# Performance work log

Measured on AMD Instinct MI355X. Metric: run time of the kernel, lower is better.

The kernel has to match this reference:

```python
import jax, jax.numpy as jnp
import numpy as np

N_NODES = 100000
F_DIM = 128
D_LAT = 64
N_EDGES = 1000000
H_DIM = 128


def setup_inputs() -> dict:
    key = jax.random.key(0)
    ks = jax.random.split(key, 10)
    rng = np.random.default_rng(0)
    # positive edges (random graph) and non-edge negative pairs (dedup vs edge set,
    # mirroring the membership check in the torch elbo loop)
    edges = rng.integers(0, N_NODES, size=(2, N_EDGES))
    edge_hash = edges[0].astype(np.int64) * N_NODES + edges[1]
    cand = rng.integers(0, N_NODES, size=(2, 2 * N_EDGES))
    cand_hash = cand[0].astype(np.int64) * N_NODES + cand[1]
    keep = ~np.isin(cand_hash, edge_hash)
    neg = cand[:, keep][:, :N_EDGES]
    r = lambda k, s, sc=1.0: jax.random.normal(k, s, jnp.float32) * sc
    return {
        "x": r(ks[0], (N_NODES, F_DIM)),
        "eps": r(ks[1], (N_NODES, D_LAT)),
        "W_mu": r(ks[2], (F_DIM, D_LAT), 0.05),
        "b_mu": jnp.zeros((D_LAT,), jnp.float32),
        "W_lv": r(ks[3], (F_DIM, D_LAT), 0.05),
        "b_lv": jnp.zeros((D_LAT,), jnp.float32),
        "W1": r(ks[4], (D_LAT, H_DIM), 0.1),
        "b1": jnp.zeros((H_DIM,), jnp.float32),
        "W2": r(ks[5], (H_DIM, 1), 0.1),
        "b2": jnp.zeros((1,), jnp.float32),
        "edge_index": jnp.asarray(edges, jnp.int64) if jax.config.jax_enable_x64 else jnp.asarray(edges, jnp.int32),
        "neg_index": jnp.asarray(neg, jnp.int64) if jax.config.jax_enable_x64 else jnp.asarray(neg, jnp.int32),
    }


def reference(x, eps, W_mu, b_mu, W_lv, b_lv, W1, b1, W2, b2, edge_index, neg_index):
    # encoder: per-node diagonal Gaussian q(z|x)
    mu = x @ W_mu + b_mu            # [N, D]
    logvar = x @ W_lv + b_lv        # [N, D]
    z = mu + eps * jnp.exp(0.5 * logvar)  # q.rsample()

    def pair_logits(idx):
        zu = z[idx[0]]              # [E, D] gather
        zv = z[idx[1]]
        h = jax.nn.relu((zu * zv) @ W1 + b1)  # [E, H]
        return (h @ W2 + b2)[:, 0]  # [E]

    # Bernoulli(logits).log_prob(1) = log_sigmoid(l); log(1 - sigmoid(l)) = log_sigmoid(-l)
    true_lp = jax.nn.log_sigmoid(pair_logits(edge_index))
    false_lp = jax.nn.log_sigmoid(-pair_logits(neg_index))
    recon = jnp.mean(jnp.concatenate([true_lp, false_lp]))

    # KL(q || N(0, I)) per node, mean over nodes
    kl = jnp.mean(0.5 * jnp.sum(jnp.square(mu) + jnp.exp(logvar) - 1.0 - logvar, axis=-1))
    return -(recon - kl)
```

## Files before the change

### kernel.cpp

```cpp
#include <hip/hip_runtime.h>
#include <math.h>

#define F_DIM 128
#define D_LAT 64
#define H_DIM 128

typedef __attribute__((ext_vector_type(8))) short bf16x8;
typedef __attribute__((ext_vector_type(4))) float f32x4;
typedef __attribute__((ext_vector_type(2))) float f32x2;
typedef __attribute__((ext_vector_type(2))) unsigned long long u64x2;

__device__ __forceinline__ unsigned short f2bf(float f) {
    unsigned int u = __builtin_bit_cast(unsigned int, f);
    return (unsigned short)((u + 0x8000u) >> 16);
}

__device__ __forceinline__ long prod_fp8(unsigned long long qu, unsigned long long qv) {
    const unsigned int ul = (unsigned int)qu, uh = (unsigned int)(qu >> 32);
    const unsigned int vl = (unsigned int)qv, vh = (unsigned int)(qv >> 32);
    const f32x2 u01 = __builtin_amdgcn_cvt_pk_f32_fp8(ul, false);
    const f32x2 u23 = __builtin_amdgcn_cvt_pk_f32_fp8(ul, true);
    const f32x2 u45 = __builtin_amdgcn_cvt_pk_f32_fp8(uh, false);
    const f32x2 u67 = __builtin_amdgcn_cvt_pk_f32_fp8(uh, true);
    const f32x2 v01 = __builtin_amdgcn_cvt_pk_f32_fp8(vl, false);
    const f32x2 v23 = __builtin_amdgcn_cvt_pk_f32_fp8(vl, true);
    const f32x2 v45 = __builtin_amdgcn_cvt_pk_f32_fp8(vh, false);
    const f32x2 v67 = __builtin_amdgcn_cvt_pk_f32_fp8(vh, true);
    const f32x2 p01 = u01 * v01, p23 = u23 * v23;
    const f32x2 p45 = u45 * v45, p67 = u67 * v67;
    unsigned int r0 = __builtin_amdgcn_cvt_pk_fp8_f32(p01[0], p01[1], 0u, false);
    r0 = __builtin_amdgcn_cvt_pk_fp8_f32(p23[0], p23[1], r0, true);
    unsigned int r1 = __builtin_amdgcn_cvt_pk_fp8_f32(p45[0], p45[1], 0u, false);
    r1 = __builtin_amdgcn_cvt_pk_fp8_f32(p67[0], p67[1], r1, true);
    return (long)(((unsigned long long)r1 << 32) | r0);
}

__global__ __launch_bounds__(256) void enc_mfma_kernel(
    const float* __restrict__ x, const float* __restrict__ eps,
    const float* __restrict__ Wmu, const float* __restrict__ bmu,
    const float* __restrict__ Wlv, const float* __restrict__ blv,
    unsigned char* __restrict__ zb, float* __restrict__ accum, int nNodes)
{
    const int lane = threadIdx.x & 63;
    const int li   = lane & 15;
    const int gi   = lane >> 4;

    bf16x8 wf[8][4];
#pragma unroll
    for (int t = 0; t < 4; ++t)
#pragma unroll
        for (int s = 0; s < 4; ++s)
#pragma unroll
            for (int j = 0; j < 8; ++j) {
                const int k = s * 32 + gi * 8 + j;
                wf[t][s][j]     = (short)f2bf(Wmu[k * D_LAT + 16 * t + li]);
                wf[t + 4][s][j] = (short)f2bf(Wlv[k * D_LAT + 16 * t + li]);
            }
    float bmu4[4], blv4[4];
#pragma unroll
    for (int t = 0; t < 4; ++t) {
        bmu4[t] = bmu[16 * t + li];
        blv4[t] = blv[16 * t + li];
    }

    const int wid = (blockIdx.x * blockDim.x + threadIdx.x) >> 6;
    const int nw  = (gridDim.x * blockDim.x) >> 6;
    const int NB  = nNodes >> 4;

    float klacc = 0.f;
    for (int nb = wid; nb < NB; nb += nw) {
        const int nbase = nb << 4;
        const float* __restrict__ xrow = x + (size_t)(nbase + li) * F_DIM;

        bf16x8 af[4];
#pragma unroll
        for (int s = 0; s < 4; ++s) {
            const f32x4 v0 = *(const f32x4*)(xrow + s * 32 + gi * 8);
            const f32x4 v1 = *(const f32x4*)(xrow + s * 32 + gi * 8 + 4);
#pragma unroll
            for (int j = 0; j < 4; ++j) {
                af[s][j]     = (short)f2bf(v0[j]);
                af[s][j + 4] = (short)f2bf(v1[j]);
            }
        }

        f32x4 acc[8];
#pragma unroll
        for (int t = 0; t < 4; ++t) {
            acc[t]     = (f32x4){bmu4[t], bmu4[t], bmu4[t], bmu4[t]};
            acc[t + 4] = (f32x4){blv4[t], blv4[t], blv4[t], blv4[t]};
        }
#pragma unroll
        for (int t = 0; t < 8; ++t)
#pragma unroll
            for (int s = 0; s < 4; ++s)
                acc[t] = __builtin_amdgcn_mfma_f32_16x16x32_bf16(af[s], wf[t][s], acc[t], 0, 0, 0);

#pragma unroll
        for (int r = 0; r < 4; ++r) {
            const int row = nbase + gi * 4 + r;
#pragma unroll
            for (int t = 0; t < 4; ++t) {
                const float mu  = acc[t][r];
                const float lv  = acc[t + 4][r];
                const float e05 = __expf(0.5f * lv);
                klacc += mu * mu + e05 * e05 - 1.0f - lv;
                const float zv = fmaf(eps[(size_t)row * D_LAT + 16 * t + li], e05, mu);
                zb[(size_t)row * D_LAT + 16 * t + li] =
                    (unsigned char)(__builtin_amdgcn_cvt_pk_fp8_f32(zv, 0.f, 0u, false) & 0xffu);
            }
        }
    }
    for (int off = 32; off; off >>= 1) klacc += __shfl_xor(klacc, off);
    if (lane == 0) atomicAdd(&accum[1], 0.5f * klacc);
}

__global__ __launch_bounds__(256) void edge_mfma_kernel(
    const unsigned char* __restrict__ zb,
    const int* __restrict__ eidx, const int* __restrict__ nidx,
    const float* __restrict__ W1, const float* __restrict__ b1,
    const float* __restrict__ W2, const float* __restrict__ b2,
    float* __restrict__ accum, int E)
{
    const int lane = threadIdx.x & 63;
    const int li   = lane & 15;
    const int gi   = lane >> 4;

    long w1q[8][2];
#pragma unroll
    for (int t = 0; t < 8; ++t)
#pragma unroll
        for (int s = 0; s < 2; ++s) {
            float f[8];
#pragma unroll
            for (int j = 0; j < 8; ++j)
                f[j] = W1[(gi * 16 + s * 8 + j) * H_DIM + 16 * t + li];
            unsigned int r0 = __builtin_amdgcn_cvt_pk_fp8_f32(f[0], f[1], 0u, false);
            r0 = __builtin_amdgcn_cvt_pk_fp8_f32(f[2], f[3], r0, true);
            unsigned int r1 = __builtin_amdgcn_cvt_pk_fp8_f32(f[4], f[5], 0u, false);
            r1 = __builtin_amdgcn_cvt_pk_fp8_f32(f[6], f[7], r1, true);
            w1q[t][s] = (long)(((unsigned long long)r1 << 32) | r0);
        }
    float b1r[8], w2r[8];
#pragma unroll
    for (int t = 0; t < 8; ++t) {
        b1r[t] = b1[16 * t + li];
        w2r[t] = W2[16 * t + li];
    }
    const float b2v = b2[0];

    const int wid = (blockIdx.x * blockDim.x + threadIdx.x) >> 6;
    const int nw  = (gridDim.x * blockDim.x) >> 6;
    const int NBpos = E >> 4;
    const int NBH   = NBpos;

    float lp = 0.f;

    auto load_idx = [&](int hb, int& u0, int& v0, int& u1, int& v1) {
        const int h   = (hb < NBH) ? hb : (NBH - 1);
        const int pb0 = 2 * h, pb1 = 2 * h + 1;
        const int* __restrict__ i0 = (pb0 < NBpos) ? eidx : nidx;
        const int* __restrict__ i1 = (pb1 < NBpos) ? eidx : nidx;
        const int m0 = ((pb0 < NBpos) ? pb0 : pb0 - NBpos) << 4;
        const int m1 = ((pb1 < NBpos) ? pb1 : pb1 - NBpos) << 4;
        u0 = i0[m0 + li]; v0 = i0[E + m0 + li];
        u1 = i1[m1 + li]; v1 = i1[E + m1 + li];
    };
    auto load_row = [&](int node) -> u64x2 {
        return *(const u64x2*)(zb + (size_t)node * D_LAT + (gi << 4));
    };
    auto do_block = [&](u64x2 qu, u64x2 qv, bool pos) {
        const long pa0 = prod_fp8(qu[0], qv[0]);
        const long pa1 = prod_fp8(qu[1], qv[1]);
        f32x4 acc[8];
#pragma unroll
        for (int t = 0; t < 8; ++t)
            acc[t] = (f32x4){b1r[t], b1r[t], b1r[t], b1r[t]};
#pragma unroll
        for (int t = 0; t < 8; ++t) {
            acc[t] = __builtin_amdgcn_mfma_f32_16x16x32_fp8_fp8(pa0, w1q[t][0], acc[t], 0, 0, 0);
            acc[t] = __builtin_amdgcn_mfma_f32_16x16x32_fp8_fp8(pa1, w1q[t][1], acc[t], 0, 0, 0);
        }
        float t0 = 0.f, t1 = 0.f, t2 = 0.f, t3 = 0.f;
#pragma unroll
        for (int t = 0; t < 8; ++t) {
            t0 += fmaxf(acc[t][0], 0.f) * w2r[t];
            t1 += fmaxf(acc[t][1], 0.f) * w2r[t];
            t2 += fmaxf(acc[t][2], 0.f) * w2r[t];
            t3 += fmaxf(acc[t][3], 0.f) * w2r[t];
        }
#pragma unroll
        for (int off = 1; off < 16; off <<= 1) {
            t0 += __shfl_xor(t0, off);
            t1 += __shfl_xor(t1, off);
            t2 += __shfl_xor(t2, off);
            t3 += __shfl_xor(t3, off);
        }
        const float sg = pos ? 1.f : -1.f;
        const float l0 = sg * (t0 + b2v), l1 = sg * (t1 + b2v);
        const float l2 = sg * (t2 + b2v), l3 = sg * (t3 + b2v);
        lp += fminf(l0, 0.f) - __logf(1.f + __expf(-fabsf(l0)));
        lp += fminf(l1, 0.f) - __logf(1.f + __expf(-fabsf(l1)));
        lp += fminf(l2, 0.f) - __logf(1.f + __expf(-fabsf(l2)));
        lp += fminf(l3, 0.f) - __logf(1.f + __expf(-fabsf(l3)));
    };

    int ju0, jv0, ju1, jv1;
    load_idx(wid, ju0, jv0, ju1, jv1);
    u64x2 A0u = load_row(ju0), A0v = load_row(jv0);
    u64x2 A1u = load_row(ju1), A1v = load_row(jv1);
    load_idx(wid + nw, ju0, jv0, ju1, jv1);

#pragma unroll 2
    for (int hb = wid; hb < NBH; hb += nw) {
        u64x2 B0u = load_row(ju0), B0v = load_row(jv0);
        u64x2 B1u = load_row(ju1), B1v = load_row(jv1);
        int ku0, kv0, ku1, kv1;
        load_idx(hb + 2 * nw, ku0, kv0, ku1, kv1);
        do_block(A0u, A0v, 2 * hb < NBpos);
        do_block(A1u, A1v, 2 * hb + 1 < NBpos);
        A0u = B0u; A0v = B0v; A1u = B1u; A1v = B1v;
        ju0 = ku0; jv0 = kv0; ju1 = ku1; jv1 = kv1;
    }

    for (int off = 32; off; off >>= 1) lp += __shfl_xor(lp, off);
    if (lane == 0) atomicAdd(&accum[0], lp * 0.0625f);
}

__global__ void fin_kernel(const float* __restrict__ accum, float* __restrict__ out,
                           int nNodes, int E)
{
    const float recon = accum[0] / (float)(2 * E);
    const float kl    = accum[1] / (float)nNodes;
    out[0] = kl - recon;
}

extern "C" void kernel_launch(void* const* d_in, const int* in_sizes, int n_in,
                              void* d_out, int out_size, void* d_ws, size_t ws_size,
                              hipStream_t stream)
{
    const float* x    = (const float*)d_in[0];
    const float* eps  = (const float*)d_in[1];
    const float* Wmu  = (const float*)d_in[2];
    const float* bmu  = (const float*)d_in[3];
    const float* Wlv  = (const float*)d_in[4];
    const float* blv  = (const float*)d_in[5];
    const float* W1   = (const float*)d_in[6];
    const float* b1   = (const float*)d_in[7];
    const float* W2   = (const float*)d_in[8];
    const float* b2   = (const float*)d_in[9];
    const int*   eidx = (const int*)d_in[10];
    const int*   nidx = (const int*)d_in[11];

    const int nNodes = in_sizes[1] / D_LAT;
    const int E      = in_sizes[10] / 2;

    float* accum      = (float*)d_ws;
    unsigned char* zb = (unsigned char*)((char*)d_ws + 256);

    hipMemsetAsync(d_ws, 0, 256, stream);
    enc_mfma_kernel<<<512, 256, 0, stream>>>(x, eps, Wmu, bmu, Wlv, blv, zb, accum, nNodes);
    edge_mfma_kernel<<<2048, 256, 0, stream>>>(zb, eidx, nidx, W1, b1, W2, b2, accum, E);
    fin_kernel<<<1, 1, 0, stream>>>(accum, (float*)d_out, nNodes, E);
}
```

Baseline: 202.4 us.

## Stage gathered latent rows into LDS via async global_load_lds double buffering

Replaces the register-prefetched gathers of z rows with direct global-to-LDS async loads (16 bytes per lane) into a per-wave double buffer. Indices are prefetched three steps ahead and rows two steps ahead, with explicit vmcnt and lgkmcnt waits. The aim is to keep more gather requests in flight and hide gather latency behind the MFMA work. In exchange it adds LDS traffic, LDS reads and hand-written waitcnt synchronisation. The lane-to-LDS layout must also match the original per-lane row slices.

```diff
diff --git a/kernel.cpp b/kernel.cpp
--- a/kernel.cpp
+++ b/kernel.cpp
@@ -14,6 +14,11 @@
     unsigned int u = __builtin_bit_cast(unsigned int, f);
     return (unsigned short)((u + 0x8000u) >> 16);
 }
+
+#define GLDS16(gaddr, laddr)                                                        \
+    __builtin_amdgcn_global_load_lds(                                               \
+        (const __attribute__((address_space(1))) void*)(gaddr),                     \
+        (__attribute__((address_space(3))) void*)(laddr), 16, 0, 0)
 
 __device__ __forceinline__ long prod_fp8(unsigned long long qu, unsigned long long qv) {
     const unsigned int ul = (unsigned int)qu, uh = (unsigned int)(qu >> 32);
@@ -122,9 +127,12 @@
     const float* __restrict__ W2, const float* __restrict__ b2,
     float* __restrict__ accum, int E)
 {
+    __shared__ unsigned char sh[4][2][4][1024];
+
     const int lane = threadIdx.x & 63;
     const int li   = lane & 15;
     const int gi   = lane >> 4;
+    const int w    = threadIdx.x >> 6;
 
     long w1q[8][2];
 #pragma unroll
@@ -166,8 +174,11 @@
         u0 = i0[m0 + li]; v0 = i0[E + m0 + li];
         u1 = i1[m1 + li]; v1 = i1[E + m1 + li];
     };
-    auto load_row = [&](int node) -> u64x2 {
-        return *(const u64x2*)(zb + (size_t)node * D_LAT + (gi << 4));
+    auto stage = [&](int slot, int u0, int v0, int u1, int v1) {
+        GLDS16(zb + (size_t)u0 * D_LAT + (gi << 4), &sh[w][slot][0][0]);
+        GLDS16(zb + (size_t)v0 * D_LAT + (gi << 4), &sh[w][slot][1][0]);
+        GLDS16(zb + (size_t)u1 * D_LAT + (gi << 4), &sh[w][slot][2][0]);
+        GLDS16(zb + (size_t)v1 * D_LAT + (gi << 4), &sh[w][slot][3][0]);
     };
     auto do_block = [&](u64x2 qu, u64x2 qv, bool pos) {
         const long pa0 = prod_fp8(qu[0], qv[0]);
@@ -205,22 +216,30 @@
         lp += fminf(l3, 0.f) - __logf(1.f + __expf(-fabsf(l3)));
     };
 
-    int ju0, jv0, ju1, jv1;
-    load_idx(wid, ju0, jv0, ju1, jv1);
-    u64x2 A0u = load_row(ju0), A0v = load_row(jv0);
-    u64x2 A1u = load_row(ju1), A1v = load_row(jv1);
-    load_idx(wid + nw, ju0, jv0, ju1, jv1);
-
-#pragma unroll 2
-    for (int hb = wid; hb < NBH; hb += nw) {
-        u64x2 B0u = load_row(ju0), B0v = load_row(jv0);
-        u64x2 B1u = load_row(ju1), B1v = load_row(jv1);
-        int ku0, kv0, ku1, kv1;
-        load_idx(hb + 2 * nw, ku0, kv0, ku1, kv1);
-        do_block(A0u, A0v, 2 * hb < NBpos);
-        do_block(A1u, A1v, 2 * hb + 1 < NBpos);
-        A0u = B0u; A0v = B0v; A1u = B1u; A1v = B1v;
-        ju0 = ku0; jv0 = kv0; ju1 = ku1; jv1 = kv1;
+    int iu0, iv0, iu1, iv1;
+    load_idx(wid, iu0, iv0, iu1, iv1);
+    stage(0, iu0, iv0, iu1, iv1);
+    load_idx(wid + nw, iu0, iv0, iu1, iv1);
+    stage(1, iu0, iv0, iu1, iv1);
+    load_idx(wid + 2 * nw, iu0, iv0, iu1, iv1);
+
+    int slot = 0;
+    for (int hb = wid; hb < NBH; hb += nw, slot ^= 1) {
+        asm volatile("s_waitcnt vmcnt(8)" ::: "memory");
+        const unsigned char* base = &sh[w][slot][0][0];
+        const u64x2 qu0 = *(const u64x2*)(base + (lane << 4));
+        const u64x2 qv0 = *(const u64x2*)(base + 1024 + (lane << 4));
+        const u64x2 qu1 = *(const u64x2*)(base + 2048 + (lane << 4));
+        const u64x2 qv1 = *(const u64x2*)(base + 3072 + (lane << 4));
+        asm volatile("s_waitcnt lgkmcnt(0)" ::: "memory");
+
+        int ju0, jv0, ju1, jv1;
+        load_idx(hb + 3 * nw, ju0, jv0, ju1, jv1);
+        stage(slot, iu0, iv0, iu1, iv1);
+        iu0 = ju0; iv0 = jv0; iu1 = ju1; iv1 = jv1;
+
+        do_block(qu0, qv0, 2 * hb < NBpos);
+        do_block(qu1, qv1, 2 * hb + 1 < NBpos);
     }
 
     for (int off = 32; off; off >>= 1) lp += __shfl_xor(lp, off);
```

Result: slower. 212.1 us (+4.8%).
